# Kernel tuning notes

Measured on AMD Instinct MI355X. Metric: run time of the kernel, lower is better.

Reference implementation:

```python
import jax, jax.numpy as jnp
import numpy as np

B, T, C = 2, 2048, 1024
N_HEAD = 16
G_NON = 32   # qgroup_size_non (layernorm / residual path)
G_LIN = 32   # qgroup_size_lin (linear path)
QMAX = 127.0
EPS = 1e-5


def quantize(x, G):
    """Group-wise symmetric int8 quantization along the last dim.
    Returns q (int8, same shape as x) and scales s with shape x.shape[:-1] + (D//G,)."""
    shp = x.shape
    xg = x.reshape(shp[:-1] + (shp[-1] // G, G))
    s = jnp.maximum(jnp.max(jnp.abs(xg), axis=-1) / QMAX, 1e-8)
    q = jnp.clip(jnp.round(xg / s[..., None]), -QMAX, QMAX).astype(jnp.int8)
    return q.reshape(shp), s


def dequant(q, s, G):
    shp = q.shape
    xg = q.astype(jnp.float32).reshape(shp[:-1] + (shp[-1] // G, G)) * s[..., None]
    return xg.reshape(shp)


def quant_dequant(x, G):
    """Fake-quantize (straight-through): forward = dequant(quantize(x))."""
    q, s = quantize(x, G)
    xd = dequant(q, s, G)
    return x + jax.lax.stop_gradient(xd - x)


def setup_inputs() -> dict:
    key = jax.random.key(0)
    k1, k2, k3, k4 = jax.random.split(key, 4)
    x = jax.random.normal(k1, (B, T, C), dtype=jnp.float32)
    # LN stats of x, produced by the previous block's int8_add_..._MeanVar
    mean = jnp.mean(x, axis=-1)
    rstd = 1.0 / jnp.sqrt(jnp.var(x, axis=-1) + EPS)
    qx, sx = quantize(x, G_NON)
    ln_w = 1.0 + 0.02 * jax.random.normal(k2, (C,), dtype=jnp.float32)
    w1 = 0.02 * jax.random.normal(k3, (3 * C, C), dtype=jnp.float32)   # c_attn.weight [out,in]
    w2 = 0.02 * jax.random.normal(k4, (C, C), dtype=jnp.float32)       # c_proj.weight [out,in]
    return {"x": x, "qx": qx.astype(jnp.int32), "sx": sx, "mean": mean,
            "rstd": rstd, "ln_w": ln_w, "w1": w1, "w2": w2}


def reference(x, qx, sx, mean, rstd, ln_w, w1, w2):
    hd = C // N_HEAD
    # ---- Part1: int8 layernorm (uses provided mean/rstd) + int8 c_attn linear ----
    ln_in = dequant(qx.astype(jnp.int8), sx, G_NON)               # [B,T,C]
    h = (ln_in - mean[..., None]) * rstd[..., None] * ln_w        # layernorm output
    hq = quant_dequant(h, G_NON)                                  # requantize activations
    w1q = quant_dequant(w1, G_LIN)                                # int8 weight
    qkv = jnp.einsum('btc,oc->bto', hq, w1q)                      # [B,T,3C]
    q, k, v = jnp.split(qkv, 3, axis=-1)
    q = q.reshape(B, T, N_HEAD, hd).transpose(0, 2, 1, 3)         # [B,H,T,hd]
    k = k.reshape(B, T, N_HEAD, hd).transpose(0, 2, 1, 3)
    v = v.reshape(B, T, N_HEAD, hd).transpose(0, 2, 1, 3)
    # ---- causal SDPA ----
    scores = jnp.einsum('bhqd,bhkd->bhqk', q, k) / jnp.sqrt(jnp.float32(hd))
    causal = jnp.tril(jnp.ones((T, T), dtype=bool))
    scores = jnp.where(causal, scores, jnp.float32(-1e30))
    attn = jax.nn.softmax(scores, axis=-1)
    y = jnp.einsum('bhqk,bhkd->bhqd', attn, v)
    y = y.transpose(0, 2, 1, 3).reshape(B, T, C)
    # ---- Part2: int8 c_proj linear + residual add with mean/var ----
    yq = quant_dequant(y, G_LIN)
    w2q = quant_dequant(w2, G_LIN)
    proj = jnp.einsum('btc,oc->bto', yq, w2q)
    fpx = x + proj                                                # fp residual output
    mean_o = jnp.mean(fpx, axis=-1)
    rstd_o = 1.0 / jnp.sqrt(jnp.var(fpx, axis=-1) + EPS)
    qo, so = quantize(fpx, G_NON)                                 # quantized output for next block
    return (fpx, qo, so, mean_o, rstd_o)
```

## Files before the change

### kernel.cpp

```cpp
#include <hip/hip_runtime.h>
#include <stdint.h>

#define BB 2
#define TT 2048
#define CC 1024
#define NH 16
#define HD 64
#define NG 32
#define ROWS (BB*TT)
#define C3 (3*CC)

typedef _Float16 half_t;
typedef __attribute__((ext_vector_type(8))) _Float16 half8;
typedef __attribute__((ext_vector_type(2))) __fp16 fp16x2;
typedef __attribute__((ext_vector_type(4))) float f32x4;

#define GLDS16(g, l) __builtin_amdgcn_global_load_lds( \
    (__attribute__((address_space(1))) void*)(g), \
    (__attribute__((address_space(3))) void*)(l), 16, 0, 0)

#define LOG2E 1.44269504f
#define DEFER_THR 5.5451774f

__device__ __forceinline__ uint32_t pk_h2(float a, float b) {
  union { fp16x2 h; uint32_t u; } cv;
  cv.h = __builtin_amdgcn_cvt_pkrtz(a, b);
  return cv.u;
}

__global__ void k_qdq_w(const float* __restrict__ w1, const float* __restrict__ w2,
                        half_t* __restrict__ o1, half_t* __restrict__ o2) {
  int g = blockIdx.x * blockDim.x + threadIdx.x;
  const float* src; half_t* dst; int gl;
  if (g < C3 * NG) { src = w1; dst = o1; gl = g; }
  else             { src = w2; dst = o2; gl = g - C3 * NG; }
  const float4* p = reinterpret_cast<const float4*>(src + (size_t)gl * 32);
  float v[32]; float amax = 0.f;
  #pragma unroll
  for (int i = 0; i < 8; ++i) {
    float4 t = p[i];
    v[4*i] = t.x; v[4*i+1] = t.y; v[4*i+2] = t.z; v[4*i+3] = t.w;
    amax = fmaxf(amax, fmaxf(fmaxf(fabsf(t.x), fabsf(t.y)), fmaxf(fabsf(t.z), fabsf(t.w))));
  }
  float s = fmaxf(amax / 127.0f, 1e-8f);
  half_t* o = dst + (size_t)gl * 32;
  #pragma unroll
  for (int c = 0; c < 4; ++c) {
    half8 ov;
    #pragma unroll
    for (int jj = 0; jj < 8; ++jj) {
      float q = fminf(fmaxf(rintf(v[c*8+jj] / s), -127.f), 127.f);
      ov[jj] = (half_t)(q * s);
    }
    *reinterpret_cast<half8*>(o + c*8) = ov;
  }
}

__global__ void k_qh(const int* __restrict__ qx, const float* __restrict__ sx,
                     const float* __restrict__ mean, const float* __restrict__ rstd,
                     const float* __restrict__ lnw, half_t* __restrict__ h16) {
  int g = blockIdx.x * blockDim.x + threadIdx.x;
  if (g >= ROWS * NG) return;
  int row = g >> 5, grp = g & 31;
  float sxv = sx[g];
  float mu = mean[row], rs = rstd[row];
  const int4* qp = reinterpret_cast<const int4*>(qx + (size_t)row * CC + grp * 32);
  const float4* wp = reinterpret_cast<const float4*>(lnw + grp * 32);
  float v[32]; float amax = 0.f;
  #pragma unroll
  for (int i = 0; i < 8; ++i) {
    int4 qv = qp[i]; float4 wv = wp[i];
    float h0 = ((float)qv.x * sxv - mu) * rs * wv.x;
    float h1 = ((float)qv.y * sxv - mu) * rs * wv.y;
    float h2 = ((float)qv.z * sxv - mu) * rs * wv.z;
    float h3 = ((float)qv.w * sxv - mu) * rs * wv.w;
    v[4*i] = h0; v[4*i+1] = h1; v[4*i+2] = h2; v[4*i+3] = h3;
    amax = fmaxf(amax, fmaxf(fmaxf(fabsf(h0), fabsf(h1)), fmaxf(fabsf(h2), fabsf(h3))));
  }
  float s = fmaxf(amax / 127.0f, 1e-8f);
  half_t* o = h16 + (size_t)row * CC + grp * 32;
  #pragma unroll
  for (int c = 0; c < 4; ++c) {
    half8 ov;
    #pragma unroll
    for (int jj = 0; jj < 8; ++jj) {
      float q = fminf(fmaxf(rintf(v[c*8+jj] / s), -127.f), 127.f);
      ov[jj] = (half_t)(q * s);
    }
    *reinterpret_cast<half8*>(o + c*8) = ov;
  }
}

template<typename TO>
__global__ __launch_bounds__(256) void k_gemm16(const half_t* __restrict__ A,
                                                const half_t* __restrict__ B,
                                                TO* __restrict__ Out, int N) {
  __shared__ __align__(16) half_t As[128*32];
  __shared__ __align__(16) half_t Bs[128*32];
  const int tid = threadIdx.x;
  const int wave = tid >> 6, lane = tid & 63;
  const int l15 = lane & 15, lg = lane >> 4;
  const int m0 = blockIdx.y * 128, n0 = blockIdx.x * 128;
  const int wm = (wave >> 1) * 64, wn = (wave & 1) * 64;
  f32x4 acc[4][4];
  #pragma unroll
  for (int i = 0; i < 4; ++i)
    #pragma unroll
    for (int jj = 0; jj < 4; ++jj) acc[i][jj] = f32x4{0.f, 0.f, 0.f, 0.f};
  const int srow = lane >> 2;
  const int scol = (lane & 3) * 8;
  const int seg0 = wave * 2;
  for (int k0 = 0; k0 < 1024; k0 += 32) {
    #pragma unroll
    for (int s = 0; s < 2; ++s) {
      const int seg = seg0 + s;
      GLDS16(A + (size_t)(m0 + seg*16 + srow) * 1024 + k0 + scol, As + seg*512);
      GLDS16(B + (size_t)(n0 + seg*16 + srow) * 1024 + k0 + scol, Bs + seg*512);
    }
    __syncthreads();
    half8 af[4], bf[4];
    #pragma unroll
    for (int i = 0; i < 4; ++i) {
      af[i] = *reinterpret_cast<const half8*>(As + (wm + i*16 + l15)*32 + lg*8);
      bf[i] = *reinterpret_cast<const half8*>(Bs + (wn + i*16 + l15)*32 + lg*8);
    }
    #pragma unroll
    for (int mi = 0; mi < 4; ++mi)
      #pragma unroll
      for (int ni = 0; ni < 4; ++ni)
        acc[mi][ni] = __builtin_amdgcn_mfma_f32_16x16x32_f16(af[mi], bf[ni], acc[mi][ni], 0, 0, 0);
    __syncthreads();
  }
  const int crow = m0 + wm + lg * 4;
  const int ccol = n0 + wn + l15;
  #pragma unroll
  for (int mi = 0; mi < 4; ++mi)
    #pragma unroll
    for (int ni = 0; ni < 4; ++ni)
      #pragma unroll
      for (int r = 0; r < 4; ++r)
        Out[(size_t)(crow + mi*16 + r) * N + ccol + ni*16] = (TO)acc[mi][ni][r];
}

__global__ __launch_bounds__(256) void k_attn16(const half_t* __restrict__ qkv,
                                                half_t* __restrict__ y16) {
  __shared__ __align__(16) half_t Ks[64*72];
  __shared__ __align__(16) half_t Vt[64*72];
  __shared__ __align__(16) half_t PsA[4][16*72];
  __shared__ __align__(16) half_t PsB[4][16*72];
  const int tid = threadIdx.x;
  const int wave = tid >> 6, lane = tid & 63;
  const int l15 = lane & 15, lg = lane >> 4;
  const int bh = blockIdx.x, b = bh >> 4, h = bh & 15;
  const int j = blockIdx.y;
  const int qtA = j, qtB = 31 - j;

  const size_t rowA = (size_t)(b * TT + qtA * 64 + wave * 16 + l15);
  const size_t rowB = (size_t)(b * TT + qtB * 64 + wave * 16 + l15);
  const half_t* qpA = qkv + rowA * C3 + h * HD + lg * 8;
  const half_t* qpB = qkv + rowB * C3 + h * HD + lg * 8;
  const half8 qa0 = *reinterpret_cast<const half8*>(qpA)      * (half_t)0.125f;
  const half8 qa1 = *reinterpret_cast<const half8*>(qpA + 32) * (half_t)0.125f;
  const half8 qb0 = *reinterpret_cast<const half8*>(qpB)      * (half_t)0.125f;
  const half8 qb1 = *reinterpret_cast<const half8*>(qpB + 32) * (half_t)0.125f;

  float mA = -3.0e38f, mB = -3.0e38f;
  f32x4 ya[4], yb[4];
  f32x4 laA = f32x4{0,0,0,0}, laB = f32x4{0,0,0,0};
  #pragma unroll
  for (int n = 0; n < 4; ++n) { ya[n] = f32x4{0,0,0,0}; yb[n] = f32x4{0,0,0,0}; }

  const int sj = tid >> 2, sc = (tid & 3) * 16;
  const int vk = (tid >> 3) * 2, vd0 = (tid & 7) * 8;
  const int vxor = ((vd0 >> 3) & 7) << 2;
  const int kp2 = vk >> 1;
  half_t* pwA = &PsA[wave][0];
  half_t* pwB = &PsB[wave][0];
  uint32_t* vt32 = reinterpret_cast<uint32_t*>(Vt);

  int vdw0[4], vdw1[4];
  #pragma unroll
  for (int n = 0; n < 4; ++n) {
    const int d = n*16 + l15;
    const int x = ((n*2 + (l15 >> 3)) & 7) << 2;
    vdw0[n] = (d*36 + lg*4) ^ x;
    vdw1[n] = (d*36 + 16 + lg*4) ^ x;
  }

  half8 ones8;
  #pragma unroll
  for (int i = 0; i < 8; ++i) ones8[i] = (half_t)1.0f;

  half8 k0r, k1r; uint4 u0r, u1r;
  const half_t* kvb = qkv + ((size_t)b * TT) * C3 + CC + h * HD;
  auto kload = [&](int kt) {
    const half_t* kp = kvb + (size_t)(kt*64 + sj) * C3 + sc;
    k0r = *reinterpret_cast<const half8*>(kp);
    k1r = *reinterpret_cast<const half8*>(kp + 8);
    const half_t* vp = kvb + (size_t)(kt*64 + vk) * C3 + CC + vd0;
    u0r = *reinterpret_cast<const uint4*>(vp);
    u1r = *reinterpret_cast<const uint4*>(vp + C3);
  };

  auto qkt = [&](f32x4* sacc, const half8 q0, const half8 q1) {
    __builtin_amdgcn_s_setprio(1);
    #pragma unroll
    for (int kg = 0; kg < 4; ++kg) {
      const half8 a0 = *reinterpret_cast<const half8*>(Ks + (kg*16 + l15)*72 + lg*8);
      const half8 a1 = *reinterpret_cast<const half8*>(Ks + (kg*16 + l15)*72 + lg*8 + 32);
      f32x4 t = f32x4{0,0,0,0};
      t = __builtin_amdgcn_mfma_f32_16x16x32_f16(a0, q0, t, 0, 0, 0);
      t = __builtin_amdgcn_mfma_f32_16x16x32_f16(a1, q1, t, 0, 0, 0);
      sacc[kg] = t;
    }
    __builtin_amdgcn_s_setprio(0);
  };

  auto finish = [&](f32x4* sacc, bool diag, half_t* pw,
                    float& m, f32x4& lacc, f32x4* yacc) {
    float sv[16]; float tm = -3.0e38f;
    #pragma unroll
    for (int kg = 0; kg < 4; ++kg)
      #pragma unroll
      for (int r = 0; r < 4; ++r) {
        float s = sacc[kg][r];
        if (diag && (kg*16 + lg*4 + r > wave*16 + l15)) s = -1e30f;
        sv[kg*4 + r] = s;
        tm = fmaxf(tm, s);
      }
    tm = fmaxf(tm, __shfl_xor(tm, 16));
    tm = fmaxf(tm, __shfl_xor(tm, 32));
    if (!__all(tm <= m + DEFER_THR)) {
      const float mn = fmaxf(m, tm);
      const float alpha = __builtin_amdgcn_exp2f((m - mn) * LOG2E);
      #pragma unroll
      for (int n = 0; n < 4; ++n) yacc[n] *= alpha;
      lacc *= alpha;
      m = mn;
    }
    const float nm = -m * LOG2E;
    #pragma unroll
    for (int i = 0; i < 16; ++i)
      sv[i] = __builtin_amdgcn_exp2f(fmaf(sv[i], LOG2E, nm));
    uint32_t* pd = reinterpret_cast<uint32_t*>(pw) + l15*36 + lg*2;
    #pragma unroll
    for (int kg = 0; kg < 4; ++kg) {
      pd[kg*8 + 0] = pk_h2(sv[kg*4 + 0], sv[kg*4 + 1]);
      pd[kg*8 + 1] = pk_h2(sv[kg*4 + 2], sv[kg*4 + 3]);
    }
    __builtin_amdgcn_sched_barrier(0);
    const half8 pb0 = *reinterpret_cast<const half8*>(pw + l15*72 + lg*8);
    const half8 pb1 = *reinterpret_cast<const half8*>(pw + l15*72 + lg*8 + 32);
    __builtin_amdgcn_s_setprio(1);
    #pragma unroll
    for (int n = 0; n < 4; ++n) {
      const half8 va0 = *reinterpret_cast<const half8*>(vt32 + vdw0[n]);
      const half8 va1 = *reinterpret_cast<const half8*>(vt32 + vdw1[n]);
      yacc[n] = __builtin_amdgcn_mfma_f32_16x16x32_f16(va0, pb0, yacc[n], 0, 0, 0);
      yacc[n] = __builtin_amdgcn_mfma_f32_16x16x32_f16(va1, pb1, yacc[n], 0, 0, 0);
    }
    lacc = __builtin_amdgcn_mfma_f32_16x16x32_f16(ones8, pb0, lacc, 0, 0, 0);
    lacc = __builtin_amdgcn_mfma_f32_16x16x32_f16(ones8, pb1, lacc, 0, 0, 0);
    __builtin_amdgcn_s_setprio(0);
  };

  kload(0);
  for (int kt = 0; kt <= qtB; ++kt) {
    __syncthreads();
    *reinterpret_cast<half8*>(Ks + sj*72 + sc) = k0r;
    *reinterpret_cast<half8*>(Ks + sj*72 + sc + 8) = k1r;
    {
      const uint32_t w0[4] = {u0r.x, u0r.y, u0r.z, u0r.w};
      const uint32_t w1[4] = {u1r.x, u1r.y, u1r.z, u1r.w};
      #pragma unroll
      for (int i = 0; i < 4; ++i) {
        const int d = vd0 + 2*i;
        vt32[(d*36 + kp2) ^ vxor]       = __builtin_amdgcn_perm(w1[i], w0[i], 0x05040100u);
        vt32[((d+1)*36 + kp2) ^ vxor]   = __builtin_amdgcn_perm(w1[i], w0[i], 0x07060302u);
      }
    }
    __syncthreads();
    if (kt < qtB) kload(kt + 1);
    const bool actA = (kt <= qtA);
    f32x4 sB[4], sA[4];
    qkt(sB, qb0, qb1);
    if (actA) qkt(sA, qa0, qa1);
    finish(sB, kt == qtB, pwB, mB, laB, yb);
    if (actA) finish(sA, kt == qtA, pwA, mA, laA, ya);
  }

  auto epi = [&](size_t row, float l, f32x4* yacc) {
    const float inv = 1.0f / l;
    float v[16];
    #pragma unroll
    for (int n = 0; n < 4; ++n)
      #pragma unroll
      for (int r = 0; r < 4; ++r) v[n*4 + r] = yacc[n][r] * inv;
    half_t* yp = y16 + row * CC + h * HD;
    #pragma unroll
    for (int g = 0; g < 2; ++g) {
      float am = 0.f;
      #pragma unroll
      for (int t = 0; t < 8; ++t) am = fmaxf(am, fabsf(v[g*8 + t]));
      am = fmaxf(am, __shfl_xor(am, 16));
      am = fmaxf(am, __shfl_xor(am, 32));
      const float s = fmaxf(am / 127.0f, 1e-8f);
      const float qi = 1.0f / s;
      #pragma unroll
      for (int nn = 0; nn < 2; ++nn) {
        const int n = g*2 + nn;
        union { half_t h4[4]; uint64_t u; } pk;
        #pragma unroll
        for (int r = 0; r < 4; ++r) {
          float q = fminf(fmaxf(rintf(v[n*4 + r] * qi), -127.f), 127.f);
          pk.h4[r] = (half_t)(q * s);
        }
        *reinterpret_cast<uint64_t*>(yp + n*16 + lg*4) = pk.u;
      }
    }
  };
  epi(rowB, laB[0], yb);
  epi(rowA, laA[0], ya);
}

__global__ __launch_bounds__(256) void k_final(
    const float* __restrict__ x, const half_t* __restrict__ proj,
    float* __restrict__ out_fpx, float* __restrict__ out_qo, float* __restrict__ out_so,
    float* __restrict__ out_mean, float* __restrict__ out_rstd) {
  __shared__ float red[16];
  int row = blockIdx.x;
  int tid = threadIdx.x;
  size_t base = (size_t)row * CC + tid * 4;
  float4 xv = *reinterpret_cast<const float4*>(x + base);
  union { uint64_t u; half_t h[4]; } pp;
  pp.u = *reinterpret_cast<const uint64_t*>(proj + base);
  float4 f;
  f.x = xv.x + (float)pp.h[0]; f.y = xv.y + (float)pp.h[1];
  f.z = xv.z + (float)pp.h[2]; f.w = xv.w + (float)pp.h[3];
  *reinterpret_cast<float4*>(out_fpx + base) = f;
  float sum = f.x + f.y + f.z + f.w;
  float sq  = f.x*f.x + f.y*f.y + f.z*f.z + f.w*f.w;
  #pragma unroll
  for (int off = 1; off < 64; off <<= 1) {
    sum += __shfl_xor(sum, off);
    sq  += __shfl_xor(sq, off);
  }
  int wid = tid >> 6, lane = tid & 63;
  if (lane == 0) { red[wid] = sum; red[8 + wid] = sq; }
  __syncthreads();
  if (tid == 0) {
    float s4 = red[0] + red[1] + red[2] + red[3];
    float q4 = red[8] + red[9] + red[10] + red[11];
    float mu = s4 * (1.0f / CC);
    float var = q4 * (1.0f / CC) - mu * mu;
    out_mean[row] = mu;
    out_rstd[row] = 1.0f / sqrtf(var + 1e-5f);
  }
  float amax = fmaxf(fmaxf(fabsf(f.x), fabsf(f.y)), fmaxf(fabsf(f.z), fabsf(f.w)));
  #pragma unroll
  for (int off = 1; off < 8; off <<= 1) amax = fmaxf(amax, __shfl_xor(amax, off, 8));
  float s = fmaxf(amax / 127.0f, 1e-8f);
  int g = tid >> 3, li = tid & 7;
  if (li == 0) out_so[row * NG + g] = s;
  float4 qo;
  qo.x = fminf(fmaxf(rintf(f.x / s), -127.f), 127.f);
  qo.y = fminf(fmaxf(rintf(f.y / s), -127.f), 127.f);
  qo.z = fminf(fmaxf(rintf(f.z / s), -127.f), 127.f);
  qo.w = fminf(fmaxf(rintf(f.w / s), -127.f), 127.f);
  *reinterpret_cast<float4*>(out_qo + base) = qo;
}

extern "C" void kernel_launch(void* const* d_in, const int* in_sizes, int n_in,
                              void* d_out, int out_size, void* d_ws, size_t ws_size,
                              hipStream_t stream) {
  const float* x    = (const float*)d_in[0];
  const int*   qx   = (const int*)d_in[1];
  const float* sx   = (const float*)d_in[2];
  const float* mean = (const float*)d_in[3];
  const float* rstd = (const float*)d_in[4];
  const float* lnw  = (const float*)d_in[5];
  const float* w1   = (const float*)d_in[6];
  const float* w2   = (const float*)d_in[7];

  float* out = (float*)d_out;
  float* o_fpx  = out;
  float* o_qo   = o_fpx + (size_t)ROWS * CC;
  float* o_so   = o_qo  + (size_t)ROWS * CC;
  float* o_mean = o_so  + (size_t)ROWS * NG;
  float* o_rstd = o_mean + ROWS;

  size_t off = 0;
  char* wsb = (char*)d_ws;
  auto alloc = [&](size_t bytes) -> void* {
    void* p = wsb + off;
    off += (bytes + 255) & ~(size_t)255;
    return p;
  };
  half_t* h16   = (half_t*)alloc((size_t)ROWS * CC * 2);
  half_t* w116  = (half_t*)alloc((size_t)C3 * CC * 2);
  half_t* w216  = (half_t*)alloc((size_t)CC * CC * 2);
  half_t* qkv16 = (half_t*)alloc((size_t)ROWS * C3 * 2);
  half_t* y16   = (half_t*)alloc((size_t)ROWS * CC * 2);
  half_t* proj  = (half_t*)alloc((size_t)ROWS * CC * 2);

  k_qdq_w<<<(C3 * NG + CC * NG) / 256, 256, 0, stream>>>(w1, w2, w116, w216);
  k_qh<<<(ROWS * NG) / 256, 256, 0, stream>>>(qx, sx, mean, rstd, lnw, h16);
  k_gemm16<half_t><<<dim3(C3 / 128, ROWS / 128), 256, 0, stream>>>(h16, w116, qkv16, C3);
  k_attn16<<<dim3(BB * NH, 16), 256, 0, stream>>>(qkv16, y16);
  k_gemm16<half_t><<<dim3(CC / 128, ROWS / 128), 256, 0, stream>>>(y16, w216, proj, CC);
  k_final<<<ROWS, 256, 0, stream>>>(x, proj, o_fpx, o_qo, o_so, o_mean, o_rstd);
}
```

Measured before the change: 132.7 us.

## Split paired causal query tiles across 8 waves in attention kernel

The attention block now launches 512 threads, and waves 0-3 and 4-7 each own one of the two paired query tiles (j and 31-j). Before, each of 4 waves processed both tiles in sequence. This cuts per-wave register state and serial work, and lets more waves hide latency. K/V staging is now spread over 512 threads with smaller per-thread loads. The cost is that the j-tile waves sit idle, waiting at the barriers, once their causal range ends, and occupancy is limited by launch bounds (512, 4).

```diff
diff --git a/kernel.cpp b/kernel.cpp
--- a/kernel.cpp
+++ b/kernel.cpp
@@ -142,40 +142,35 @@
         Out[(size_t)(crow + mi*16 + r) * N + ccol + ni*16] = (TO)acc[mi][ni][r];
 }
 
-__global__ __launch_bounds__(256) void k_attn16(const half_t* __restrict__ qkv,
-                                                half_t* __restrict__ y16) {
+__global__ __launch_bounds__(512, 4) void k_attn16(const half_t* __restrict__ qkv,
+                                                   half_t* __restrict__ y16) {
   __shared__ __align__(16) half_t Ks[64*72];
   __shared__ __align__(16) half_t Vt[64*72];
-  __shared__ __align__(16) half_t PsA[4][16*72];
-  __shared__ __align__(16) half_t PsB[4][16*72];
+  __shared__ __align__(16) half_t Ps[8][16*72];
   const int tid = threadIdx.x;
   const int wave = tid >> 6, lane = tid & 63;
   const int l15 = lane & 15, lg = lane >> 4;
+  const int w4 = wave & 3;
   const int bh = blockIdx.x, b = bh >> 4, h = bh & 15;
   const int j = blockIdx.y;
-  const int qtA = j, qtB = 31 - j;
-
-  const size_t rowA = (size_t)(b * TT + qtA * 64 + wave * 16 + l15);
-  const size_t rowB = (size_t)(b * TT + qtB * 64 + wave * 16 + l15);
-  const half_t* qpA = qkv + rowA * C3 + h * HD + lg * 8;
-  const half_t* qpB = qkv + rowB * C3 + h * HD + lg * 8;
-  const half8 qa0 = *reinterpret_cast<const half8*>(qpA)      * (half_t)0.125f;
-  const half8 qa1 = *reinterpret_cast<const half8*>(qpA + 32) * (half_t)0.125f;
-  const half8 qb0 = *reinterpret_cast<const half8*>(qpB)      * (half_t)0.125f;
-  const half8 qb1 = *reinterpret_cast<const half8*>(qpB + 32) * (half_t)0.125f;
-
-  float mA = -3.0e38f, mB = -3.0e38f;
-  f32x4 ya[4], yb[4];
-  f32x4 laA = f32x4{0,0,0,0}, laB = f32x4{0,0,0,0};
-  #pragma unroll
-  for (int n = 0; n < 4; ++n) { ya[n] = f32x4{0,0,0,0}; yb[n] = f32x4{0,0,0,0}; }
-
-  const int sj = tid >> 2, sc = (tid & 3) * 16;
-  const int vk = (tid >> 3) * 2, vd0 = (tid & 7) * 8;
+  const int qtB = 31 - j;
+  const int qt = (wave >> 2) ? qtB : j;
+
+  const size_t row = (size_t)(b * TT + qt * 64 + w4 * 16 + l15);
+  const half_t* qp = qkv + row * C3 + h * HD + lg * 8;
+  const half8 q0 = *reinterpret_cast<const half8*>(qp)      * (half_t)0.125f;
+  const half8 q1 = *reinterpret_cast<const half8*>(qp + 32) * (half_t)0.125f;
+
+  float m = -3.0e38f;
+  f32x4 yacc[4];
+  f32x4 lacc = f32x4{0,0,0,0};
+  #pragma unroll
+  for (int n = 0; n < 4; ++n) yacc[n] = f32x4{0,0,0,0};
+
+  const int sj = tid >> 3, sc = (tid & 7) * 8;
+  const int vkp = tid >> 4, vd0 = (tid & 15) * 4;
   const int vxor = ((vd0 >> 3) & 7) << 2;
-  const int kp2 = vk >> 1;
-  half_t* pwA = &PsA[wave][0];
-  half_t* pwB = &PsB[wave][0];
+  half_t* pw = &Ps[wave][0];
   uint32_t* vt32 = reinterpret_cast<uint32_t*>(Vt);
 
   int vdw0[4], vdw1[4];
@@ -191,136 +186,117 @@
   #pragma unroll
   for (int i = 0; i < 8; ++i) ones8[i] = (half_t)1.0f;
 
-  half8 k0r, k1r; uint4 u0r, u1r;
+  half8 k0r; uint2 u0r, u1r;
   const half_t* kvb = qkv + ((size_t)b * TT) * C3 + CC + h * HD;
   auto kload = [&](int kt) {
     const half_t* kp = kvb + (size_t)(kt*64 + sj) * C3 + sc;
     k0r = *reinterpret_cast<const half8*>(kp);
-    k1r = *reinterpret_cast<const half8*>(kp + 8);
-    const half_t* vp = kvb + (size_t)(kt*64 + vk) * C3 + CC + vd0;
-    u0r = *reinterpret_cast<const uint4*>(vp);
-    u1r = *reinterpret_cast<const uint4*>(vp + C3);
-  };
-
-  auto qkt = [&](f32x4* sacc, const half8 q0, const half8 q1) {
-    __builtin_amdgcn_s_setprio(1);
-    #pragma unroll
-    for (int kg = 0; kg < 4; ++kg) {
-      const half8 a0 = *reinterpret_cast<const half8*>(Ks + (kg*16 + l15)*72 + lg*8);
-      const half8 a1 = *reinterpret_cast<const half8*>(Ks + (kg*16 + l15)*72 + lg*8 + 32);
-      f32x4 t = f32x4{0,0,0,0};
-      t = __builtin_amdgcn_mfma_f32_16x16x32_f16(a0, q0, t, 0, 0, 0);
-      t = __builtin_amdgcn_mfma_f32_16x16x32_f16(a1, q1, t, 0, 0, 0);
-      sacc[kg] = t;
-    }
-    __builtin_amdgcn_s_setprio(0);
-  };
-
-  auto finish = [&](f32x4* sacc, bool diag, half_t* pw,
-                    float& m, f32x4& lacc, f32x4* yacc) {
-    float sv[16]; float tm = -3.0e38f;
-    #pragma unroll
-    for (int kg = 0; kg < 4; ++kg)
-      #pragma unroll
-      for (int r = 0; r < 4; ++r) {
-        float s = sacc[kg][r];
-        if (diag && (kg*16 + lg*4 + r > wave*16 + l15)) s = -1e30f;
-        sv[kg*4 + r] = s;
-        tm = fmaxf(tm, s);
-      }
-    tm = fmaxf(tm, __shfl_xor(tm, 16));
-    tm = fmaxf(tm, __shfl_xor(tm, 32));
-    if (!__all(tm <= m + DEFER_THR)) {
-      const float mn = fmaxf(m, tm);
-      const float alpha = __builtin_amdgcn_exp2f((m - mn) * LOG2E);
-      #pragma unroll
-      for (int n = 0; n < 4; ++n) yacc[n] *= alpha;
-      lacc *= alpha;
-      m = mn;
-    }
-    const float nm = -m * LOG2E;
-    #pragma unroll
-    for (int i = 0; i < 16; ++i)
-      sv[i] = __builtin_amdgcn_exp2f(fmaf(sv[i], LOG2E, nm));
-    uint32_t* pd = reinterpret_cast<uint32_t*>(pw) + l15*36 + lg*2;
-    #pragma unroll
-    for (int kg = 0; kg < 4; ++kg) {
-      pd[kg*8 + 0] = pk_h2(sv[kg*4 + 0], sv[kg*4 + 1]);
-      pd[kg*8 + 1] = pk_h2(sv[kg*4 + 2], sv[kg*4 + 3]);
-    }
-    __builtin_amdgcn_sched_barrier(0);
-    const half8 pb0 = *reinterpret_cast<const half8*>(pw + l15*72 + lg*8);
-    const half8 pb1 = *reinterpret_cast<const half8*>(pw + l15*72 + lg*8 + 32);
-    __builtin_amdgcn_s_setprio(1);
-    #pragma unroll
-    for (int n = 0; n < 4; ++n) {
-      const half8 va0 = *reinterpret_cast<const half8*>(vt32 + vdw0[n]);
-      const half8 va1 = *reinterpret_cast<const half8*>(vt32 + vdw1[n]);
-      yacc[n] = __builtin_amdgcn_mfma_f32_16x16x32_f16(va0, pb0, yacc[n], 0, 0, 0);
-      yacc[n] = __builtin_amdgcn_mfma_f32_16x16x32_f16(va1, pb1, yacc[n], 0, 0, 0);
-    }
-    lacc = __builtin_amdgcn_mfma_f32_16x16x32_f16(ones8, pb0, lacc, 0, 0, 0);
-    lacc = __builtin_amdgcn_mfma_f32_16x16x32_f16(ones8, pb1, lacc, 0, 0, 0);
-    __builtin_amdgcn_s_setprio(0);
+    const half_t* vp = kvb + (size_t)(kt*64 + vkp*2) * C3 + CC + vd0;
+    u0r = *reinterpret_cast<const uint2*>(vp);
+    u1r = *reinterpret_cast<const uint2*>(vp + C3);
   };
 
   kload(0);
   for (int kt = 0; kt <= qtB; ++kt) {
     __syncthreads();
     *reinterpret_cast<half8*>(Ks + sj*72 + sc) = k0r;
-    *reinterpret_cast<half8*>(Ks + sj*72 + sc + 8) = k1r;
-    {
-      const uint32_t w0[4] = {u0r.x, u0r.y, u0r.z, u0r.w};
-      const uint32_t w1[4] = {u1r.x, u1r.y, u1r.z, u1r.w};
-      #pragma unroll
-      for (int i = 0; i < 4; ++i) {
-        const int d = vd0 + 2*i;
-        vt32[(d*36 + kp2) ^ vxor]       = __builtin_amdgcn_perm(w1[i], w0[i], 0x05040100u);
-        vt32[((d+1)*36 + kp2) ^ vxor]   = __builtin_amdgcn_perm(w1[i], w0[i], 0x07060302u);
-      }
-    }
+    vt32[((vd0+0)*36 + vkp) ^ vxor] = __builtin_amdgcn_perm(u1r.x, u0r.x, 0x05040100u);
+    vt32[((vd0+1)*36 + vkp) ^ vxor] = __builtin_amdgcn_perm(u1r.x, u0r.x, 0x07060302u);
+    vt32[((vd0+2)*36 + vkp) ^ vxor] = __builtin_amdgcn_perm(u1r.y, u0r.y, 0x05040100u);
+    vt32[((vd0+3)*36 + vkp) ^ vxor] = __builtin_amdgcn_perm(u1r.y, u0r.y, 0x07060302u);
     __syncthreads();
     if (kt < qtB) kload(kt + 1);
-    const bool actA = (kt <= qtA);
-    f32x4 sB[4], sA[4];
-    qkt(sB, qb0, qb1);
-    if (actA) qkt(sA, qa0, qa1);
-    finish(sB, kt == qtB, pwB, mB, laB, yb);
-    if (actA) finish(sA, kt == qtA, pwA, mA, laA, ya);
-  }
-
-  auto epi = [&](size_t row, float l, f32x4* yacc) {
-    const float inv = 1.0f / l;
-    float v[16];
-    #pragma unroll
-    for (int n = 0; n < 4; ++n)
-      #pragma unroll
-      for (int r = 0; r < 4; ++r) v[n*4 + r] = yacc[n][r] * inv;
-    half_t* yp = y16 + row * CC + h * HD;
-    #pragma unroll
-    for (int g = 0; g < 2; ++g) {
-      float am = 0.f;
-      #pragma unroll
-      for (int t = 0; t < 8; ++t) am = fmaxf(am, fabsf(v[g*8 + t]));
-      am = fmaxf(am, __shfl_xor(am, 16));
-      am = fmaxf(am, __shfl_xor(am, 32));
-      const float s = fmaxf(am / 127.0f, 1e-8f);
-      const float qi = 1.0f / s;
-      #pragma unroll
-      for (int nn = 0; nn < 2; ++nn) {
-        const int n = g*2 + nn;
-        union { half_t h4[4]; uint64_t u; } pk;
+    if (kt <= qt) {
+      f32x4 sacc[4];
+      __builtin_amdgcn_s_setprio(1);
+      #pragma unroll
+      for (int kg = 0; kg < 4; ++kg) {
+        const half8 a0 = *reinterpret_cast<const half8*>(Ks + (kg*16 + l15)*72 + lg*8);
+        const half8 a1 = *reinterpret_cast<const half8*>(Ks + (kg*16 + l15)*72 + lg*8 + 32);
+        f32x4 t = f32x4{0,0,0,0};
+        t = __builtin_amdgcn_mfma_f32_16x16x32_f16(a0, q0, t, 0, 0, 0);
+        t = __builtin_amdgcn_mfma_f32_16x16x32_f16(a1, q1, t, 0, 0, 0);
+        sacc[kg] = t;
+      }
+      __builtin_amdgcn_s_setprio(0);
+      float sv[16]; float tm = -3.0e38f;
+      const bool diag = (kt == qt);
+      #pragma unroll
+      for (int kg = 0; kg < 4; ++kg)
         #pragma unroll
         for (int r = 0; r < 4; ++r) {
-          float q = fminf(fmaxf(rintf(v[n*4 + r] * qi), -127.f), 127.f);
-          pk.h4[r] = (half_t)(q * s);
+          float s = sacc[kg][r];
+          if (diag && (kg*16 + lg*4 + r > w4*16 + l15)) s = -1e30f;
+          sv[kg*4 + r] = s;
+          tm = fmaxf(tm, s);
         }
-        *reinterpret_cast<uint64_t*>(yp + n*16 + lg*4) = pk.u;
-      }
-    }
-  };
-  epi(rowB, laB[0], yb);
-  epi(rowA, laA[0], ya);
+      tm = fmaxf(tm, __shfl_xor(tm, 16));
+      tm = fmaxf(tm, __shfl_xor(tm, 32));
+      if (!__all(tm <= m + DEFER_THR)) {
+        const float mn = fmaxf(m, tm);
+        const float alpha = __builtin_amdgcn_exp2f((m - mn) * LOG2E);
+        #pragma unroll
+        for (int n = 0; n < 4; ++n) yacc[n] *= alpha;
+        lacc *= alpha;
+        m = mn;
+      }
+      const float nm = -m * LOG2E;
+      #pragma unroll
+      for (int i = 0; i < 16; ++i)
+        sv[i] = __builtin_amdgcn_exp2f(fmaf(sv[i], LOG2E, nm));
+      uint32_t* pd = reinterpret_cast<uint32_t*>(pw) + l15*36 + lg*2;
+      #pragma unroll
+      for (int kg = 0; kg < 4; ++kg) {
+        uint2 pr;
+        pr.x = pk_h2(sv[kg*4 + 0], sv[kg*4 + 1]);
+        pr.y = pk_h2(sv[kg*4 + 2], sv[kg*4 + 3]);
+        *reinterpret_cast<uint2*>(pd + kg*8) = pr;
+      }
+      __builtin_amdgcn_sched_barrier(0);
+      const half8 pb0 = *reinterpret_cast<const half8*>(pw + l15*72 + lg*8);
+      const half8 pb1 = *reinterpret_cast<const half8*>(pw + l15*72 + lg*8 + 32);
+      __builtin_amdgcn_s_setprio(1);
+      #pragma unroll
+      for (int n = 0; n < 4; ++n) {
+        const half8 va0 = *reinterpret_cast<const half8*>(vt32 + vdw0[n]);
+        const half8 va1 = *reinterpret_cast<const half8*>(vt32 + vdw1[n]);
+        yacc[n] = __builtin_amdgcn_mfma_f32_16x16x32_f16(va0, pb0, yacc[n], 0, 0, 0);
+        yacc[n] = __builtin_amdgcn_mfma_f32_16x16x32_f16(va1, pb1, yacc[n], 0, 0, 0);
+      }
+      lacc = __builtin_amdgcn_mfma_f32_16x16x32_f16(ones8, pb0, lacc, 0, 0, 0);
+      lacc = __builtin_amdgcn_mfma_f32_16x16x32_f16(ones8, pb1, lacc, 0, 0, 0);
+      __builtin_amdgcn_s_setprio(0);
+    }
+  }
+
+  const float inv = 1.0f / lacc[0];
+  float v[16];
+  #pragma unroll
+  for (int n = 0; n < 4; ++n)
+    #pragma unroll
+    for (int r = 0; r < 4; ++r) v[n*4 + r] = yacc[n][r] * inv;
+  half_t* yp = y16 + row * CC + h * HD;
+  #pragma unroll
+  for (int g = 0; g < 2; ++g) {
+    float am = 0.f;
+    #pragma unroll
+    for (int t = 0; t < 8; ++t) am = fmaxf(am, fabsf(v[g*8 + t]));
+    am = fmaxf(am, __shfl_xor(am, 16));
+    am = fmaxf(am, __shfl_xor(am, 32));
+    const float s = fmaxf(am / 127.0f, 1e-8f);
+    const float qi = 1.0f / s;
+    #pragma unroll
+    for (int nn = 0; nn < 2; ++nn) {
+      const int n = g*2 + nn;
+      union { half_t h4[4]; uint64_t u; } pk;
+      #pragma unroll
+      for (int r = 0; r < 4; ++r) {
+        float q = fminf(fmaxf(rintf(v[n*4 + r] * qi), -127.f), 127.f);
+        pk.h4[r] = (half_t)(q * s);
+      }
+      *reinterpret_cast<uint64_t*>(yp + n*16 + lg*4) = pk.u;
+    }
+  }
 }
 
 __global__ __launch_bounds__(256) void k_final(
@@ -406,7 +382,7 @@
   k_qdq_w<<<(C3 * NG + CC * NG) / 256, 256, 0, stream>>>(w1, w2, w116, w216);
   k_qh<<<(ROWS * NG) / 256, 256, 0, stream>>>(qx, sx, mean, rstd, lnw, h16);
   k_gemm16<half_t><<<dim3(C3 / 128, ROWS / 128), 256, 0, stream>>>(h16, w116, qkv16, C3);
-  k_attn16<<<dim3(BB * NH, 16), 256, 0, stream>>>(qkv16, y16);
+  k_attn16<<<dim3(BB * NH, 16), 512, 0, stream>>>(qkv16, y16);
   k_gemm16<half_t><<<dim3(CC / 128, ROWS / 128), 256, 0, stream>>>(y16, w216, proj, CC);
   k_final<<<ROWS, 256, 0, stream>>>(x, proj, o_fpx, o_qo, o_so, o_mean, o_rstd);
 }
```

Result: no change. 130.6 us (-1.5%).
